# Kernel tuning notes

Measured on AMD Instinct MI355X. Metric: run time of the kernel, lower is better.

Reference implementation:

```python
import jax, jax.numpy as jnp
import numpy as np
import math

DIM = 1024
NUM_ACTIONS = 8
ACTION_BINS = 256
D_STATE = 16
D_CONV = 4
EXPAND = 2
D_INNER = EXPAND * DIM
DT_RANK = math.ceil(DIM / 16)


def setup_inputs() -> dict:
    key = jax.random.key(0)
    ks = jax.random.split(key, 12)
    b, s = 512, 64
    encoded_state = jax.random.normal(ks[0], (b, s, DIM), dtype=jnp.float32)
    actions = jax.random.randint(ks[1], (b, NUM_ACTIONS - 1), 0, ACTION_BINS)
    # module params
    action_bin_embeddings = 0.02 * jax.random.normal(ks[2], (NUM_ACTIONS, ACTION_BINS, DIM), dtype=jnp.float32)
    gamma = jnp.ones((DIM,), dtype=jnp.float32)
    # mamba params
    sc = 0.02
    in_proj_w = sc * jax.random.normal(ks[3], (2 * D_INNER, DIM), dtype=jnp.float32)
    conv_w = sc * jax.random.normal(ks[4], (D_INNER, D_CONV), dtype=jnp.float32)
    conv_b = jnp.zeros((D_INNER,), dtype=jnp.float32)
    x_proj_w = sc * jax.random.normal(ks[5], (DT_RANK + 2 * D_STATE, D_INNER), dtype=jnp.float32)
    dt_proj_w = sc * jax.random.normal(ks[6], (D_INNER, DT_RANK), dtype=jnp.float32)
    dt_proj_b = jax.random.uniform(ks[7], (D_INNER,), minval=-4.0, maxval=-2.0)
    A_log = jnp.log(jnp.broadcast_to(jnp.arange(1, D_STATE + 1, dtype=jnp.float32), (D_INNER, D_STATE)))
    D_param = jnp.ones((D_INNER,), dtype=jnp.float32)
    out_proj_w = sc * jax.random.normal(ks[8], (DIM, D_INNER), dtype=jnp.float32)
    return dict(encoded_state=encoded_state, actions=actions,
                action_bin_embeddings=action_bin_embeddings, gamma=gamma,
                in_proj_w=in_proj_w, conv_w=conv_w, conv_b=conv_b,
                x_proj_w=x_proj_w, dt_proj_w=dt_proj_w, dt_proj_b=dt_proj_b,
                A_log=A_log, D_param=D_param, out_proj_w=out_proj_w)


def selective_scan(u, delta, A, B, C, D):
    # u: [b, l, d_in], delta: [b, l, d_in], A: [d_in, n], B,C: [b, l, n], D: [d_in]
    dA = jnp.exp(jnp.einsum('bld,dn->bldn', delta, A))          # [b,l,d,n]
    dBu = jnp.einsum('bld,bln,bld->bldn', delta, B, u)           # [b,l,d,n]

    def step(h, inp):
        dA_t, dBu_t, C_t = inp
        h = dA_t * h + dBu_t                                      # [b,d,n]
        y = jnp.einsum('bdn,bn->bd', h, C_t)
        return h, y

    b, l, d = u.shape
    h0 = jnp.zeros((b, d, A.shape[1]), dtype=u.dtype)
    _, ys = jax.lax.scan(step, h0,
                         (dA.transpose(1, 0, 2, 3), dBu.transpose(1, 0, 2, 3), C.transpose(1, 0, 2)))
    y = ys.transpose(1, 0, 2)                                     # [b,l,d]
    return y + u * D


def mamba_forward(x, in_proj_w, conv_w, conv_b, x_proj_w, dt_proj_w, dt_proj_b, A_log, D_param, out_proj_w):
    # x: [b, l, dim]
    xz = jnp.einsum('bld,ed->ble', x, in_proj_w)                  # [b,l,2*d_inner]
    xh, z = jnp.split(xz, 2, axis=-1)
    # causal depthwise conv1d, kernel D_CONV, padding left
    xp = jnp.pad(xh, ((0, 0), (D_CONV - 1, 0), (0, 0)))
    # conv: out[b,t,c] = sum_k xp[b,t+k,c]*conv_w[c,k]
    xc = sum(xp[:, k:k + xh.shape[1], :] * conv_w[:, k] for k in range(D_CONV)) + conv_b
    xc = jax.nn.silu(xc)
    x_dbl = jnp.einsum('bld,ed->ble', xc, x_proj_w)
    dt, B, C = jnp.split(x_dbl, [DT_RANK, DT_RANK + D_STATE], axis=-1)
    delta = jax.nn.softplus(jnp.einsum('blr,dr->bld', dt, dt_proj_w) + dt_proj_b)
    A = -jnp.exp(A_log)
    y = selective_scan(xc, delta, A, B, C, D_param)
    y = y * jax.nn.silu(z)
    return jnp.einsum('bld,od->blo', y, out_proj_w)


def reference(encoded_state, actions, action_bin_embeddings, gamma,
              in_proj_w, conv_w, conv_b, x_proj_w, dt_proj_w, dt_proj_b,
              A_log, D_param, out_proj_w):
    b = encoded_state.shape[0]
    sos = jnp.mean(encoded_state, axis=tuple(range(1, encoded_state.ndim - 1)), keepdims=False)[:, None, :]  # [b,1,d]
    n = actions.shape[1]
    # gather bin embeddings: action_bin_embeddings[i, actions[b,i]] -> [b,n,d]
    bin_emb = jnp.take_along_axis(
        jnp.broadcast_to(action_bin_embeddings[:n], (b, n, ACTION_BINS, DIM)),
        actions[:, :, None, None].astype(jnp.int32).repeat(1, axis=2),
        axis=2)[:, :, 0, :]
    tokens = jnp.concatenate([sos, bin_emb], axis=1)[:, :NUM_ACTIONS]    # [b, num_actions, d]
    embed = mamba_forward(tokens, in_proj_w, conv_w, conv_b, x_proj_w,
                          dt_proj_w, dt_proj_b, A_log, D_param, out_proj_w)
    num_actions = embed.shape[-2]
    abe = jnp.roll(action_bin_embeddings[:num_actions], shift=-1, axis=1)  # [n,a,d]
    logits = jnp.einsum('bnd,nad->bna', embed, abe)
    return jax.nn.sigmoid(logits)
```

## Files before the change

kernel.cpp:

```cpp
#include <hip/hip_runtime.h>
#include <hip/hip_bf16.h>
#include <math.h>

#define DIM 1024
#define NUM_ACTIONS 8
#define ACTION_BINS 256
#define D_STATE 16
#define D_CONV 4
#define D_INNER 2048
#define DT_RANK 64
#define BATCH 512
#define SEQ 64
#define NTOK (BATCH * NUM_ACTIONS)

typedef __attribute__((ext_vector_type(8))) short short8;
typedef __attribute__((ext_vector_type(4))) float floatx4;

__device__ __forceinline__ unsigned short f2bf(float f) {
    unsigned int u = __float_as_uint(f);
    unsigned int rnd = 0x7fffu + ((u >> 16) & 1u);
    return (unsigned short)((u + rnd) >> 16);
}
__device__ __forceinline__ float bf2f(unsigned short v) {
    return __uint_as_float(((unsigned int)v) << 16);
}

__device__ __forceinline__ void async_ld16(const void* g, void* l) {
    __builtin_amdgcn_global_load_lds(
        (const __attribute__((address_space(1))) void*)g,
        (__attribute__((address_space(3))) void*)l, 16, 0, 0);
}


__global__ __launch_bounds__(256)
void sos_part(const float* __restrict__ enc, float* __restrict__ part) {
    int c = blockIdx.x;
    int b = blockIdx.y;
    int tx = threadIdx.x;
    const float4* p = (const float4*)(enc + ((size_t)b * SEQ + c * 8) * DIM) + tx;
    float4 a = make_float4(0.f, 0.f, 0.f, 0.f);
#pragma unroll
    for (int s = 0; s < 8; ++s) {
        float4 v = p[(size_t)s * (DIM / 4)];
        a.x += v.x; a.y += v.y; a.z += v.z; a.w += v.w;
    }
    ((float4*)part)[((size_t)b * 8 + c) * 256 + tx] = a;
}

#define NG0 524288
#define NG1 (NG0 + 262144)
#define NG2 (NG1 + 262144)
#define NG3 (NG2 + 16384)
#define NG4 (NG3 + 32768)
#define NPREP (NG4 + 1048576)

__device__ __forceinline__ void pack8(const float* __restrict__ src,
                                      unsigned short* __restrict__ dst) {
    float4 v0 = ((const float4*)src)[0];
    float4 v1 = ((const float4*)src)[1];
    ushort4 o0, o1;
    o0.x = f2bf(v0.x); o0.y = f2bf(v0.y); o0.z = f2bf(v0.z); o0.w = f2bf(v0.w);
    o1.x = f2bf(v1.x); o1.y = f2bf(v1.y); o1.z = f2bf(v1.z); o1.w = f2bf(v1.w);
    ((ushort4*)dst)[0] = o0; ((ushort4*)dst)[1] = o1;
}

__global__ __launch_bounds__(256)
void prep(const float* __restrict__ inw, const float* __restrict__ outw,
          const float* __restrict__ abe, const float* __restrict__ dtw,
          const float* __restrict__ xpw, const float* __restrict__ sospart,
          const int* __restrict__ actions,
          unsigned short* __restrict__ inw_pk, unsigned short* __restrict__ outw_pk,
          unsigned short* __restrict__ abe_pk, unsigned short* __restrict__ dtw_pk,
          unsigned short* __restrict__ xpw_pk, unsigned short* __restrict__ tok_pk) {
    int i = blockIdx.x * 256 + threadIdx.x;
    if (i < NG0) {
        int r = i >> 7, s = i & 127;
        pack8(inw + (size_t)r * 1024 + s * 8,
              inw_pk + (((size_t)(r >> 7) * 128 + s) << 10) + (r & 127) * 8);
    } else if (i < NG1) {
        int j = i - NG0; int r = j >> 8, s = j & 255;
        pack8(outw + (size_t)r * 2048 + s * 8,
              outw_pk + (((size_t)(r >> 7) * 256 + s) << 10) + (r & 127) * 8);
    } else if (i < NG2) {
        int j = i - NG1; int slot = j >> 15; int jj = j & 32767;
        int r = jj >> 7, s = jj & 127;
        pack8(abe + ((size_t)slot * ACTION_BINS + ((r + 1) & 255)) * 1024 + s * 8,
              abe_pk + (size_t)slot * 262144
                     + (((size_t)(r >> 7) * 128 + s) << 10) + (r & 127) * 8);
    } else if (i < NG3) {
        int j = i - NG2; int r = j >> 3, s = j & 7;
        pack8(dtw + (size_t)r * 64 + s * 8,
              dtw_pk + (((size_t)(r >> 7) * 8 + s) << 10) + (r & 127) * 8);
    } else if (i < NG4) {
        int j = i - NG3; int r = j >> 8, s = j & 255;
        unsigned short* dst = xpw_pk + ((size_t)s << 10) + (r & 127) * 8;
        if (r < 96) pack8(xpw + (size_t)r * 2048 + s * 8, dst);
        else { ushort4 z; z.x = z.y = z.z = z.w = 0;
               ((ushort4*)dst)[0] = z; ((ushort4*)dst)[1] = z; }
    } else {
        int j = i - NG4;
        int tx = j & 255;
        int t = (j >> 8) & 7;
        int b = j >> 11;
        float4 v;
        if (t == 0) {
            const float4* pp = (const float4*)sospart + (size_t)b * 8 * 256 + tx;
            float4 a = make_float4(0.f, 0.f, 0.f, 0.f);
#pragma unroll
            for (int c = 0; c < 8; ++c) {
                float4 x = pp[c * 256];
                a.x += x.x; a.y += x.y; a.z += x.z; a.w += x.w;
            }
            v = make_float4(a.x * (1.f / SEQ), a.y * (1.f / SEQ),
                            a.z * (1.f / SEQ), a.w * (1.f / SEQ));
        } else {
            int a = actions[b * (NUM_ACTIONS - 1) + (t - 1)];
            v = ((const float4*)(abe + ((size_t)(t - 1) * ACTION_BINS + a) * DIM))[tx];
        }
        int m = b * 8 + t;
        ushort4 o;
        o.x = f2bf(v.x); o.y = f2bf(v.y); o.z = f2bf(v.z); o.w = f2bf(v.w);
        size_t addr = ((size_t)(m >> 7) * 128 + (tx >> 1)) * 1024
                    + (size_t)(m & 127) * 8 + (tx & 1) * 4;
        *(ushort4*)(tok_pk + addr) = o;
    }
}

template <int MODE, int RGX, int RGY, int SKL2>
__global__ __launch_bounds__(256)
void gemm_pk(const unsigned short* __restrict__ A, long long aStride,
             const unsigned short* __restrict__ W, long long wStride,
             const float* __restrict__ aux1, const float* __restrict__ aux2,
             void* __restrict__ out1, void* __restrict__ out2,
             int ldo, long long oStride, int Ktot, int K, int Nout) {
    constexpr int SHSZ = (MODE == 5) ? 16640 : 16384;
    __shared__ alignas(16) unsigned short SH[SHSZ];
    unsigned short* As = SH;
    unsigned short* Bs = SH + 8192;

    int bx = blockIdx.x, by = blockIdx.y;
    if (RGX > 0) {
        int gx = gridDim.x;
        int id = by * gx + bx;
        constexpr int P = RGX * RGY;
        int xcd = id & 7, h = id >> 3;
        int pos = h % P, sup = h / P;
        int rgn = xcd + 8 * sup;
        int rgx_cnt = gx / RGX;
        int rm = rgn % rgx_cnt, rn = rgn / rgx_cnt;
        bx = rm * RGX + pos % RGX;
        by = rn * RGY + pos / RGX;
    }

    int kbase = 0;
    if (MODE == 7) {
        int kc = blockIdx.z & ((1 << SKL2) - 1);
        int slot = blockIdx.z >> SKL2;
        kbase = kc * K;
        A += (size_t)slot * aStride;
        W += (size_t)slot * wStride;
    }
    const int Ks = Ktot >> 3;

    int tid = threadIdx.x;
    int w = tid >> 6, l = tid & 63;
    int q = l >> 4, lan = l & 15;
    int m0 = bx * 128, n0 = by * 128;
    int wm = (w >> 1) * 64, wn = (w & 1) * 64;

    const unsigned short* gA = A + ((size_t)bx * Ks + (kbase >> 3) + 2 * w) * 1024 + l * 8;
    const unsigned short* gB = W + ((size_t)by * Ks + (kbase >> 3) + 2 * w) * 1024 + l * 8;
    unsigned short* lA = &As[2 * w * 1024];
    unsigned short* lB = &Bs[2 * w * 1024];

    floatx4 acc[4][4];
#pragma unroll
    for (int mi = 0; mi < 4; ++mi)
#pragma unroll
        for (int ni = 0; ni < 4; ++ni) acc[mi][ni] = (floatx4){0.f, 0.f, 0.f, 0.f};

    for (int k0 = 0; k0 < K; k0 += 64) {
        async_ld16(gA, lA);               async_ld16(gA + 512, lA + 512);
        async_ld16(gA + 1024, lA + 1024); async_ld16(gA + 1536, lA + 1536);
        async_ld16(gB, lB);               async_ld16(gB + 512, lB + 512);
        async_ld16(gB + 1024, lB + 1024); async_ld16(gB + 1536, lB + 1536);
        gA += 8192; gB += 8192;
        __syncthreads();

#pragma unroll
        for (int kk = 0; kk < 2; ++kk) {
            short8 a[4], b[4];
            const int ak = (q + 4 * kk) * 1024;
#pragma unroll
            for (int i = 0; i < 4; ++i)
                a[i] = *(const short8*)&As[ak + (wm + i * 16 + lan) * 8];
#pragma unroll
            for (int i = 0; i < 4; ++i)
                b[i] = *(const short8*)&Bs[ak + (wn + i * 16 + lan) * 8];
#pragma unroll
            for (int mi = 0; mi < 4; ++mi)
#pragma unroll
                for (int ni = 0; ni < 4; ++ni)
                    acc[mi][ni] = __builtin_amdgcn_mfma_f32_16x16x32_bf16(
                        a[mi], b[ni], acc[mi][ni], 0, 0, 0);
        }
        __syncthreads();
    }

    if (MODE == 5) {
        if (n0 < D_INNER) {
#pragma unroll
            for (int mi = 0; mi < 4; ++mi)
#pragma unroll
                for (int r = 0; r < 4; ++r) {
                    int tl = wm + mi * 16 + q * 4 + r;
#pragma unroll
                    for (int ni = 0; ni < 4; ++ni)
                        SH[tl * 130 + wn + ni * 16 + lan] = f2bf(acc[mi][ni][r]);
                }
            __syncthreads();
#pragma unroll
            for (int ni = 0; ni < 4; ++ni) {
                int cl = wn + ni * 16 + lan;
                int c = n0 + cl;
                float4 cw = *(const float4*)(aux1 + (size_t)c * 4);
                float cb = aux2[c];
#pragma unroll
                for (int mi = 0; mi < 4; ++mi)
#pragma unroll
                    for (int r = 0; r < 4; ++r) {
                        int tl = wm + mi * 16 + q * 4 + r;
                        int t = tl & 7;
                        float s = cb + bf2f(SH[tl * 130 + cl]) * cw.w;
                        if (t >= 1) s += bf2f(SH[(tl - 1) * 130 + cl]) * cw.z;
                        if (t >= 2) s += bf2f(SH[(tl - 2) * 130 + cl]) * cw.y;
                        if (t >= 3) s += bf2f(SH[(tl - 3) * 130 + cl]) * cw.x;
                        s = s * (1.0f / (1.0f + __expf(-s)));
                        int row = m0 + tl;
                        ((unsigned short*)out1)[((size_t)(row >> 7) * 256 + (c >> 3)) * 1024
                                                + (row & 127) * 8 + (c & 7)] = f2bf(s);
                    }
            }
        } else {
#pragma unroll
            for (int mi = 0; mi < 4; ++mi)
#pragma unroll
                for (int r = 0; r < 4; ++r) {
                    int mo = m0 + wm + mi * 16 + q * 4 + r;
#pragma unroll
                    for (int ni = 0; ni < 4; ++ni) {
                        int no = n0 + wn + ni * 16 + lan - D_INNER;
                        float v = acc[mi][ni][r];
                        float s = v * (1.0f / (1.0f + __expf(-v)));
                        ((unsigned short*)out2)[(size_t)mo * D_INNER + no] = f2bf(s);
                    }
                }
        }
    } else {
#pragma unroll
        for (int mi = 0; mi < 4; ++mi)
#pragma unroll
            for (int r = 0; r < 4; ++r) {
                int mo = m0 + wm + mi * 16 + q * 4 + r;
#pragma unroll
                for (int ni = 0; ni < 4; ++ni) {
                    int no = n0 + wn + ni * 16 + lan;
                    if (no < Nout)
                        ((float*)out1)[(size_t)blockIdx.z * oStride
                                       + (size_t)mo * ldo + no] = acc[mi][ni][r];
                }
            }
    }
}

__global__ __launch_bounds__(256)
void gemm64_pk(const unsigned short* __restrict__ A,
               const unsigned short* __restrict__ W,
               unsigned short* __restrict__ out, int Ktot, int K) {
    __shared__ alignas(16) unsigned short As[4096];
    __shared__ alignas(16) unsigned short Bs[8192];

    const int Ks = Ktot >> 3;
    int bx = blockIdx.x, by = blockIdx.y;
    int tid = threadIdx.x;
    int w = tid >> 6, l = tid & 63;
    int q = l >> 4, lan = l & 15;
    int m0 = bx * 64, n0 = by * 128;
    int wm = (w >> 1) * 32, wn = (w & 1) * 64;

    const unsigned short* gA = A + ((size_t)(bx >> 1) * Ks + 2 * w) * 1024
                                 + (bx & 1) * 512 + l * 8;
    const unsigned short* gB = W + ((size_t)by * Ks + 2 * w) * 1024 + l * 8;
    unsigned short* lA = &As[2 * w * 512];
    unsigned short* lB = &Bs[2 * w * 1024];

    floatx4 acc[2][4];
#pragma unroll
    for (int mi = 0; mi < 2; ++mi)
#pragma unroll
        for (int ni = 0; ni < 4; ++ni) acc[mi][ni] = (floatx4){0.f, 0.f, 0.f, 0.f};

    for (int k0 = 0; k0 < K; k0 += 64) {
        async_ld16(gA, lA);               async_ld16(gA + 1024, lA + 512);
        async_ld16(gB, lB);               async_ld16(gB + 512, lB + 512);
        async_ld16(gB + 1024, lB + 1024); async_ld16(gB + 1536, lB + 1536);
        gA += 8192; gB += 8192;
        __syncthreads();

#pragma unroll
        for (int kk = 0; kk < 2; ++kk) {
            short8 a[2], b[4];
            const int sA = (q + 4 * kk) * 512;
            const int sB = (q + 4 * kk) * 1024;
#pragma unroll
            for (int i = 0; i < 2; ++i)
                a[i] = *(const short8*)&As[sA + (wm + i * 16 + lan) * 8];
#pragma unroll
            for (int i = 0; i < 4; ++i)
                b[i] = *(const short8*)&Bs[sB + (wn + i * 16 + lan) * 8];
#pragma unroll
            for (int mi = 0; mi < 2; ++mi)
#pragma unroll
                for (int ni = 0; ni < 4; ++ni)
                    acc[mi][ni] = __builtin_amdgcn_mfma_f32_16x16x32_bf16(
                        a[mi], b[ni], acc[mi][ni], 0, 0, 0);
        }
        __syncthreads();
    }

#pragma unroll
    for (int mi = 0; mi < 2; ++mi)
#pragma unroll
        for (int r = 0; r < 4; ++r) {
            int mo = m0 + wm + mi * 16 + q * 4 + r;
            int slot = mo & 7, bb = mo >> 3;
#pragma unroll
            for (int ni = 0; ni < 4; ++ni) {
                int no = n0 + wn + ni * 16 + lan;
                out[(size_t)slot * 524288
                    + ((size_t)(bb >> 7) * 128 + (no >> 3)) * 1024
                    + (bb & 127) * 8 + (no & 7)] = f2bf(acc[mi][ni][r]);
            }
        }
}

__global__ __launch_bounds__(256)
void mid_kernel(const float* __restrict__ part8,
                const unsigned short* __restrict__ xc_pk,
                const unsigned short* __restrict__ zs,
                const unsigned short* __restrict__ dtw_pk,
                const float* __restrict__ dtb, const float* __restrict__ Dp,
                unsigned short* __restrict__ ys_pk) {
    int b = blockIdx.y;
    int tid = threadIdx.x;
    int d = blockIdx.x * 256 + tid;
    __shared__ float xdb[8][96];

    {
        int t = tid >> 5, n0 = tid & 31;
#pragma unroll
        for (int jj = 0; jj < 3; ++jj) {
            int n = n0 + 32 * jj;
            float s = 0.f;
#pragma unroll
            for (int z = 0; z < 8; ++z)
                s += part8[(size_t)z * (NTOK * 96) + (size_t)(b * 8 + t) * 96 + n];
            xdb[t][n] = s;
        }
    }
    __syncthreads();

    float wrow[64];
#pragma unroll
    for (int g = 0; g < 8; ++g) {
        short8 v = *(const short8*)&dtw_pk[(((size_t)(d >> 7) * 8 + g) << 10)
                                           + (size_t)(d & 127) * 8];
#pragma unroll
        for (int c2 = 0; c2 < 8; ++c2)
            wrow[g * 8 + c2] = bf2f((unsigned short)v[c2]);
    }
    float bd = dtb[d];
    float Dv = Dp[d];
    float h[D_STATE];
#pragma unroll
    for (int n = 0; n < D_STATE; ++n) h[n] = 0.f;

    size_t pbase = ((size_t)((b * 8) >> 7) * 256 + (d >> 3)) * 1024
                 + (size_t)((b * 8) & 127) * 8 + (d & 7);

    for (int t = 0; t < NUM_ACTIONS; ++t) {
        float dtv = bd;
#pragma unroll
        for (int k = 0; k < 64; ++k) dtv += xdb[t][k] * wrow[k];
        dtv = (dtv > 20.0f) ? dtv : log1pf(__expf(dtv));

        size_t po = pbase + (size_t)t * 8;
        float uu = bf2f(xc_pk[po]);
        float szv = bf2f(zs[(size_t)(b * 8 + t) * D_INNER + d]);
        float du = dtv * uu;
        float y = uu * Dv;
        float p = __expf(-dtv);
        float e = p;
#pragma unroll
        for (int n = 0; n < D_STATE; ++n) {
            h[n] = e * h[n] + du * xdb[t][64 + n];
            y += h[n] * xdb[t][80 + n];
            e *= p;
        }
        ys_pk[po] = f2bf(y * szv);
    }
}

__global__ __launch_bounds__(256)
void logits_combine(const float* __restrict__ part4, float* __restrict__ out) {
    int e = blockIdx.x * 256 + threadIdx.x;
    int slot = e >> 17;
    int rem = e & 131071;
    float s = 0.f;
#pragma unroll
    for (int kc = 0; kc < 4; ++kc)
        s += part4[((size_t)slot * 4 + kc) * 131072 + rem];
    int b = rem >> 8, bin = rem & 255;
    out[((size_t)b * 8 + slot) * 256 + bin] = 1.0f / (1.0f + __expf(-s));
}

extern "C" void kernel_launch(void* const* d_in, const int* in_sizes, int n_in,
                              void* d_out, int out_size, void* d_ws, size_t ws_size,
                              hipStream_t stream) {
    const float* enc        = (const float*)d_in[0];
    const int*   actions    = (const int*)d_in[1];
    const float* abe        = (const float*)d_in[2];
    const float* in_proj_w  = (const float*)d_in[4];
    const float* conv_w     = (const float*)d_in[5];
    const float* conv_b     = (const float*)d_in[6];
    const float* x_proj_w   = (const float*)d_in[7];
    const float* dt_proj_w  = (const float*)d_in[8];
    const float* dt_proj_b  = (const float*)d_in[9];
    const float* D_param    = (const float*)d_in[11];
    const float* out_proj_w = (const float*)d_in[12];
    float* out = (float*)d_out;

    char* p = (char*)d_ws;
    unsigned short* tok_pk  = (unsigned short*)p; p += (size_t)NTOK * DIM * 2;
    unsigned short* inw_pk  = (unsigned short*)p; p += (size_t)2 * D_INNER * DIM * 2;
    unsigned short* outw_pk = (unsigned short*)p; p += (size_t)DIM * D_INNER * 2;
    unsigned short* abe_pk  = (unsigned short*)p; p += (size_t)NUM_ACTIONS * ACTION_BINS * DIM * 2;
    unsigned short* dtw_pk  = (unsigned short*)p; p += (size_t)D_INNER * DT_RANK * 2;
    unsigned short* xpw_pk  = (unsigned short*)p; p += (size_t)128 * D_INNER * 2;
    unsigned short* xc_pk   = (unsigned short*)p; p += (size_t)NTOK * D_INNER * 2;
    unsigned short* zs      = (unsigned short*)p; p += (size_t)NTOK * D_INNER * 2;
    unsigned short* ys_pk   = (unsigned short*)p; p += (size_t)NTOK * D_INNER * 2;
    unsigned short* emb_pk  = (unsigned short*)p; p += (size_t)NTOK * DIM * 2;
    float* part8 = (float*)p; p += (size_t)8 * NTOK * 96 * 4;
    float* part4 = (float*)p; p += (size_t)32 * 512 * 256 * 4;
    float* sosp  = (float*)p; p += (size_t)BATCH * 8 * DIM * 4;

    sos_part<<<dim3(8, BATCH), 256, 0, stream>>>(enc, sosp);
    prep<<<NPREP / 256, 256, 0, stream>>>(
        in_proj_w, out_proj_w, abe, dt_proj_w, x_proj_w, sosp, actions,
        inw_pk, outw_pk, abe_pk, dtw_pk, xpw_pk, tok_pk);

    gemm_pk<5, 8, 8, 0><<<dim3(32, 32), 256, 0, stream>>>(
        tok_pk, 0, inw_pk, 0, conv_w, conv_b,
        xc_pk, zs, 0, 0, DIM, DIM, 0);

    gemm_pk<7, 0, 0, 3><<<dim3(32, 1, 8), 256, 0, stream>>>(
        xc_pk, 0, xpw_pk, 0, nullptr, nullptr,
        part8, nullptr, 96, (long long)NTOK * 96, D_INNER, D_INNER / 8, 96);

    mid_kernel<<<dim3(8, BATCH), 256, 0, stream>>>(
        part8, xc_pk, zs, dtw_pk, dt_proj_b, D_param, ys_pk);

    gemm64_pk<<<dim3(64, 8), 256, 0, stream>>>(
        ys_pk, outw_pk, emb_pk, D_INNER, D_INNER);

    gemm_pk<7, 0, 0, 2><<<dim3(4, 2, 32), 256, 0, stream>>>(
        emb_pk, 524288, abe_pk, 262144, nullptr, nullptr,
        part4, nullptr, 256, 131072, DIM, DIM / 4, 256);

    logits_combine<<<(8 * 512 * 256) / 256, 256, 0, stream>>>(part4, out);
}
```

Measured before the change: 427.3 us.

## Add 256x256-tile in_proj GEMM with fused conv/SiLU epilogue

Adds a new in_proj GEMM kernel using 256x256 output tiles, 512 threads, 128KB dynamic LDS with double-buffered async loads, interleaved MFMA phases and setprio scheduling. The causal conv and SiLU epilogue is done through shared memory, and the z half gets SiLU applied in place. The larger tiles are meant to raise data reuse and MFMA utilisation over the prior 128-tile kernel. The old path stays as a fallback if the LDS attribute cannot be set. Separately, softplus now uses fast __logf instead of log1pf, which trades a little accuracy for cheaper math.

```diff
diff --git a/kernel.cpp b/kernel.cpp
--- a/kernel.cpp
+++ b/kernel.cpp
@@ -273,6 +273,189 @@
     }
 }
 
+__global__ __launch_bounds__(512, 2)
+void gemm256_inproj(const unsigned short* __restrict__ A,
+                    const unsigned short* __restrict__ W,
+                    const float* __restrict__ cw4, const float* __restrict__ cbv,
+                    unsigned short* __restrict__ xc, unsigned short* __restrict__ zso) {
+    extern __shared__ __align__(16) unsigned short SH[];
+    unsigned short* As = SH;
+    unsigned short* Bs = SH + 32768;
+
+    const int tid = threadIdx.x;
+    const int w = tid >> 6, l = tid & 63;
+    const int q = l >> 4, lan = l & 15;
+    const int bx = blockIdx.x, by = blockIdx.y;
+    const int m0 = bx * 256, n0 = by * 256;
+    const int mh = w >> 2;
+    const int wn64 = (w & 3) * 64;
+    const int nh = wn64 >> 7;
+    const int nr0 = wn64 & 127;
+
+    const unsigned short* gA0 = A + ((size_t)(2 * bx) * 128) * 1024 + w * 1024 + l * 8;
+    const unsigned short* gA1 = gA0 + 131072;
+    const unsigned short* gB0 = W + ((size_t)(2 * by) * 128) * 1024 + w * 1024 + l * 8;
+    const unsigned short* gB1 = gB0 + 131072;
+
+    auto stageA = [&](int tt, int h) {
+        const unsigned short* g = (h ? gA1 : gA0) + (size_t)tt * 8192;
+        unsigned short* d = As + ((tt & 1) << 14) + (h << 13) + w * 1024;
+        async_ld16(g, d); async_ld16(g + 512, d + 512);
+    };
+    auto stageB = [&](int tt, int h) {
+        const unsigned short* g = (h ? gB1 : gB0) + (size_t)tt * 8192;
+        unsigned short* d = Bs + ((tt & 1) << 14) + (h << 13) + w * 1024;
+        async_ld16(g, d); async_ld16(g + 512, d + 512);
+    };
+
+    floatx4 acc[8][4];
+#pragma unroll
+    for (int mi = 0; mi < 8; ++mi)
+#pragma unroll
+        for (int ni = 0; ni < 4; ++ni) acc[mi][ni] = (floatx4){0.f, 0.f, 0.f, 0.f};
+
+    stageA(0, 0); stageA(0, 1); stageB(0, 0); stageB(0, 1);
+    stageA(1, 0); stageA(1, 1);
+
+    constexpr int NT = 16;
+#pragma unroll 2
+    for (int t = 0; t < NT; ++t) {
+        const unsigned short* Ab = As + ((t & 1) << 14) + (mh << 13);
+        const unsigned short* Bb = Bs + ((t & 1) << 14) + (nh << 13);
+        if (t + 1 < NT) asm volatile("s_waitcnt vmcnt(4)" ::: "memory");
+        else            asm volatile("s_waitcnt vmcnt(0)" ::: "memory");
+        __builtin_amdgcn_sched_barrier(0);
+        __builtin_amdgcn_s_barrier();
+
+        short8 a0[8], a1[8], b0, b1, b2, b3;
+
+#pragma unroll
+        for (int mi = 0; mi < 8; ++mi)
+            a0[mi] = *(const short8*)&Ab[q * 1024 + (mi * 16 + lan) * 8];
+        b0 = *(const short8*)&Bb[q * 1024 + (nr0 + lan) * 8];
+        b1 = *(const short8*)&Bb[q * 1024 + (nr0 + 16 + lan) * 8];
+        if (t + 1 < NT) stageB(t + 1, 0);
+        __builtin_amdgcn_s_barrier();
+        __builtin_amdgcn_s_setprio(1);
+#pragma unroll
+        for (int mi = 0; mi < 8; ++mi) {
+            acc[mi][0] = __builtin_amdgcn_mfma_f32_16x16x32_bf16(a0[mi], b0, acc[mi][0], 0, 0, 0);
+            acc[mi][1] = __builtin_amdgcn_mfma_f32_16x16x32_bf16(a0[mi], b1, acc[mi][1], 0, 0, 0);
+        }
+        __builtin_amdgcn_s_setprio(0);
+        __builtin_amdgcn_s_barrier();
+
+#pragma unroll
+        for (int mi = 0; mi < 8; ++mi)
+            a1[mi] = *(const short8*)&Ab[(4 + q) * 1024 + (mi * 16 + lan) * 8];
+        b2 = *(const short8*)&Bb[q * 1024 + (nr0 + 32 + lan) * 8];
+        b3 = *(const short8*)&Bb[q * 1024 + (nr0 + 48 + lan) * 8];
+        if (t + 1 < NT) stageB(t + 1, 1);
+        __builtin_amdgcn_s_barrier();
+        __builtin_amdgcn_s_setprio(1);
+#pragma unroll
+        for (int mi = 0; mi < 8; ++mi) {
+            acc[mi][2] = __builtin_amdgcn_mfma_f32_16x16x32_bf16(a0[mi], b2, acc[mi][2], 0, 0, 0);
+            acc[mi][3] = __builtin_amdgcn_mfma_f32_16x16x32_bf16(a0[mi], b3, acc[mi][3], 0, 0, 0);
+        }
+        __builtin_amdgcn_s_setprio(0);
+        asm volatile("s_waitcnt lgkmcnt(0)" ::: "memory");
+        __builtin_amdgcn_sched_barrier(0);
+        __builtin_amdgcn_s_barrier();
+
+        b0 = *(const short8*)&Bb[(4 + q) * 1024 + (nr0 + lan) * 8];
+        b1 = *(const short8*)&Bb[(4 + q) * 1024 + (nr0 + 16 + lan) * 8];
+        if (t + 2 < NT) stageA(t + 2, 0);
+        __builtin_amdgcn_s_barrier();
+        __builtin_amdgcn_s_setprio(1);
+#pragma unroll
+        for (int mi = 0; mi < 8; ++mi) {
+            acc[mi][0] = __builtin_amdgcn_mfma_f32_16x16x32_bf16(a1[mi], b0, acc[mi][0], 0, 0, 0);
+            acc[mi][1] = __builtin_amdgcn_mfma_f32_16x16x32_bf16(a1[mi], b1, acc[mi][1], 0, 0, 0);
+        }
+        __builtin_amdgcn_s_setprio(0);
+        __builtin_amdgcn_s_barrier();
+
+        b2 = *(const short8*)&Bb[(4 + q) * 1024 + (nr0 + 32 + lan) * 8];
+        b3 = *(const short8*)&Bb[(4 + q) * 1024 + (nr0 + 48 + lan) * 8];
+        if (t + 2 < NT) stageA(t + 2, 1);
+        __builtin_amdgcn_s_barrier();
+        __builtin_amdgcn_s_setprio(1);
+#pragma unroll
+        for (int mi = 0; mi < 8; ++mi) {
+            acc[mi][2] = __builtin_amdgcn_mfma_f32_16x16x32_bf16(a1[mi], b2, acc[mi][2], 0, 0, 0);
+            acc[mi][3] = __builtin_amdgcn_mfma_f32_16x16x32_bf16(a1[mi], b3, acc[mi][3], 0, 0, 0);
+        }
+        __builtin_amdgcn_s_setprio(0);
+    }
+
+    const int col0 = (tid & 31) * 8;
+    const int rr0 = tid >> 5;
+    if (by < 8) {
+        const int gc0 = n0 + col0;
+        float4 cwv[8]; float cbl[8];
+#pragma unroll
+        for (int j = 0; j < 8; ++j) {
+            cwv[j] = ((const float4*)cw4)[gc0 + j];
+            cbl[j] = cbv[gc0 + j];
+        }
+#pragma unroll
+        for (int hh = 0; hh < 2; ++hh) {
+            __syncthreads();
+            if (mh == hh) {
+#pragma unroll
+                for (int mi = 0; mi < 8; ++mi)
+#pragma unroll
+                    for (int ni = 0; ni < 4; ++ni)
+#pragma unroll
+                        for (int r = 0; r < 4; ++r)
+                            SH[(mi * 16 + q * 4 + r) * 264 + wn64 + ni * 16 + lan] =
+                                f2bf(acc[mi][ni][r]);
+            }
+            __syncthreads();
+#pragma unroll
+            for (int ii = 0; ii < 8; ++ii) {
+                int rr = rr0 + 16 * ii;
+                int t7 = rr & 7;
+                const unsigned short* shp = &SH[rr * 264 + col0];
+                short8 vz = {0, 0, 0, 0, 0, 0, 0, 0};
+                short8 v0 = *(const short8*)shp;
+                short8 v1 = (t7 >= 1) ? *(const short8*)(shp - 264) : vz;
+                short8 v2 = (t7 >= 2) ? *(const short8*)(shp - 528) : vz;
+                short8 v3 = (t7 >= 3) ? *(const short8*)(shp - 792) : vz;
+                short8 ov;
+#pragma unroll
+                for (int j = 0; j < 8; ++j) {
+                    float s = cbl[j]
+                            + bf2f((unsigned short)v0[j]) * cwv[j].w
+                            + bf2f((unsigned short)v1[j]) * cwv[j].z
+                            + bf2f((unsigned short)v2[j]) * cwv[j].y
+                            + bf2f((unsigned short)v3[j]) * cwv[j].x;
+                    s = s * (1.0f / (1.0f + __expf(-s)));
+                    ov[j] = (short)f2bf(s);
+                }
+                int grow = m0 + hh * 128 + rr;
+                *(short8*)&xc[(((size_t)(grow >> 7) * 256 + (gc0 >> 3)) << 10)
+                              + (size_t)(grow & 127) * 8] = ov;
+            }
+        }
+    } else {
+#pragma unroll
+        for (int mi = 0; mi < 8; ++mi)
+#pragma unroll
+            for (int r = 0; r < 4; ++r) {
+                int mo = m0 + mh * 128 + mi * 16 + q * 4 + r;
+#pragma unroll
+                for (int ni = 0; ni < 4; ++ni) {
+                    int no = n0 + wn64 + ni * 16 + lan - D_INNER;
+                    float v = acc[mi][ni][r];
+                    float s = v * (1.0f / (1.0f + __expf(-v)));
+                    zso[(size_t)mo * D_INNER + no] = f2bf(s);
+                }
+            }
+    }
+}
+
 __global__ __launch_bounds__(256)
 void gemm64_pk(const unsigned short* __restrict__ A,
                const unsigned short* __restrict__ W,
@@ -392,7 +575,7 @@
         float dtv = bd;
 #pragma unroll
         for (int k = 0; k < 64; ++k) dtv += xdb[t][k] * wrow[k];
-        dtv = (dtv > 20.0f) ? dtv : log1pf(__expf(dtv));
+        dtv = (dtv > 20.0f) ? dtv : __logf(1.0f + __expf(dtv));
 
         size_t po = pbase + (size_t)t * 8;
         float uu = bf2f(xc_pk[po]);
@@ -455,14 +638,26 @@
     float* part4 = (float*)p; p += (size_t)32 * 512 * 256 * 4;
     float* sosp  = (float*)p; p += (size_t)BATCH * 8 * DIM * 4;
 
+    static int g_bigLds = -1;
+    if (g_bigLds < 0) {
+        g_bigLds = (hipFuncSetAttribute((const void*)gemm256_inproj,
+                     hipFuncAttributeMaxDynamicSharedMemorySize, 131072)
+                    == hipSuccess) ? 1 : 0;
+    }
+
     sos_part<<<dim3(8, BATCH), 256, 0, stream>>>(enc, sosp);
     prep<<<NPREP / 256, 256, 0, stream>>>(
         in_proj_w, out_proj_w, abe, dt_proj_w, x_proj_w, sosp, actions,
         inw_pk, outw_pk, abe_pk, dtw_pk, xpw_pk, tok_pk);
 
-    gemm_pk<5, 8, 8, 0><<<dim3(32, 32), 256, 0, stream>>>(
-        tok_pk, 0, inw_pk, 0, conv_w, conv_b,
-        xc_pk, zs, 0, 0, DIM, DIM, 0);
+    if (g_bigLds) {
+        gemm256_inproj<<<dim3(16, 16), 512, 131072, stream>>>(
+            tok_pk, inw_pk, conv_w, conv_b, xc_pk, zs);
+    } else {
+        gemm_pk<5, 8, 8, 0><<<dim3(32, 32), 256, 0, stream>>>(
+            tok_pk, 0, inw_pk, 0, conv_w, conv_b,
+            xc_pk, zs, 0, 0, DIM, DIM, 0);
+    }
 
     gemm_pk<7, 0, 0, 3><<<dim3(32, 1, 8), 256, 0, stream>>>(
         xc_pk, 0, xpw_pk, 0, nullptr, nullptr,
```

Result: faster. 397.8 us (-6.9%).
